# Optimization experiments

Measured on AMD Instinct MI355X. Metric: run time of the kernel, lower is better.

## Reference

```python
import jax, jax.numpy as jnp
import numpy as np

BATCH, DIM, L, N = 2, 768, 2048, 16


def setup_inputs() -> dict:
    key = jax.random.key(0)
    ks = jax.random.split(key, 8)
    u = jax.random.normal(ks[0], (BATCH, DIM, L), dtype=jnp.float32)
    delta = jax.random.uniform(ks[1], (BATCH, DIM, L), dtype=jnp.float32)
    # A must be negative for a stable SSM (exp(delta*A) <= 1)
    A = -jax.random.uniform(ks[2], (DIM, N), dtype=jnp.float32, minval=0.5, maxval=1.5)
    B = jax.random.normal(ks[3], (BATCH, N, L), dtype=jnp.float32)
    C = jax.random.normal(ks[4], (BATCH, N, L), dtype=jnp.float32)
    D = jax.random.normal(ks[5], (DIM,), dtype=jnp.float32)
    z = jax.random.normal(ks[6], (BATCH, DIM, L), dtype=jnp.float32)
    delta_bias = 0.1 * jax.random.normal(ks[7], (DIM,), dtype=jnp.float32)
    return {"u": u, "delta": delta, "A": A, "B": B, "C": C,
            "D": D, "z": z, "delta_bias": delta_bias}


def _selective_scan(u, delta, A, B, C, D, z, delta_bias):
    # delta_softplus=True path of mamba_ssm selective_scan_fn
    delta = jax.nn.softplus(delta + delta_bias[None, :, None])  # (b, d, l)
    # discretize: deltaA = exp(delta * A), deltaB_u = delta * B * u
    deltaA = jnp.exp(jnp.einsum('bdl,dn->lbdn', delta, A))          # (l, b, d, n)
    deltaBu = jnp.einsum('bdl,bnl,bdl->lbdn', delta, B, u)          # (l, b, d, n)
    C_t = jnp.transpose(C, (2, 0, 1))                               # (l, b, n)

    def step(x, inp):
        a, bu, c = inp
        x = a * x + bu                                              # (b, d, n)
        y = jnp.einsum('bdn,bn->bd', x, c)                          # (b, d)
        return x, y

    x0 = jnp.zeros((BATCH, DIM, N), dtype=u.dtype)
    _, ys = jax.lax.scan(step, x0, (deltaA, deltaBu, C_t))          # ys: (l, b, d)
    y = jnp.transpose(ys, (1, 2, 0))                                # (b, d, l)
    out = y + u * D[None, :, None]
    out = out * jax.nn.silu(z)
    return out


def reference(u, delta, A, B, C, D, z, delta_bias):
    return _selective_scan(u, delta, A, B, C, D, z, delta_bias)
```

## Files before the change

### kernel.cpp

```cpp
#include <hip/hip_runtime.h>


#define LOG2E 1.4426950408889634f
#define LN2   0.6931471805599453f

constexpr int BATCH = 2, DIM = 768, L = 2048, N = 16;
constexpr int NC = 128, LC = 16;
constexpr int DG = DIM / 64;
constexpr int CPB = 4;
constexpr int CG = NC / CPB;
constexpr int NBLK = BATCH * DG * CG;
constexpr int NCOMB = BATCH * DIM * N;
static_assert(NC * LC == L, "chunking must cover L");

__device__ __forceinline__ float fexp2(float x) { return __builtin_amdgcn_exp2f(x); }
__device__ __forceinline__ float softplus(float v) {
  float s = LN2 * __log2f(1.0f + fexp2(v * LOG2E));
  return (v > 20.0f) ? v : s;
}
__device__ __forceinline__ float silu(float v) { return v / (1.0f + fexp2(-v * LOG2E)); }

__global__ __launch_bounds__(256, 6) void k_pass1(
    const float* __restrict__ u, const float* __restrict__ delta,
    const float* __restrict__ A, const float* __restrict__ dbias,
    const float* __restrict__ Bg, float* __restrict__ h, float* __restrict__ S)
{
  __shared__ float slab[64][68];
  __shared__ float Bsr[64][20];

  const int bid = blockIdx.x, t = threadIdx.x;
  const int cgi = bid & 31;
  const int dgb = bid >> 5;
  const int dg = dgb % DG;
  const int b = dgb / DG;
  const int d0 = dg * 64, l0 = cgi * 64;

  const int w = t >> 6, lane = t & 63;
  const int c = cgi * CPB + w;
  const int d = d0 + lane;
  const int row16 = t >> 4;
  const int col4 = (t & 15) * 4;

#pragma unroll
  for (int rr = 0; rr < 4; rr++) {
    int row = row16 + rr * 16;
    long gof = ((long)(b * DIM + d0 + row)) * L + l0 + col4;
    *(float4*)&slab[row][col4] = *(const float4*)(delta + gof);
  }
  {
    long bof = ((long)(b * N + row16)) * L + l0 + col4;
    float4 v = *(const float4*)(Bg + bof);
    Bsr[col4 + 0][row16] = v.x;
    Bsr[col4 + 1][row16] = v.y;
    Bsr[col4 + 2][row16] = v.z;
    Bsr[col4 + 3][row16] = v.w;
  }

  float A2[N];
#pragma unroll
  for (int q = 0; q < 4; q++) {
    float4 av = *(const float4*)(A + d * N + q * 4);
    A2[q*4+0] = av.x * LOG2E; A2[q*4+1] = av.y * LOG2E;
    A2[q*4+2] = av.z * LOG2E; A2[q*4+3] = av.w * LOG2E;
  }
  const float bias = dbias[d];

  __syncthreads();

  float sp[LC], Ssum = 0.f;
#pragma unroll
  for (int q = 0; q < 4; q++) {
    float4 dv = *(const float4*)&slab[lane][w * LC + q * 4];
    sp[q*4+0] = softplus(dv.x + bias);
    sp[q*4+1] = softplus(dv.y + bias);
    sp[q*4+2] = softplus(dv.z + bias);
    sp[q*4+3] = softplus(dv.w + bias);
  }
#pragma unroll
  for (int j = 0; j < LC; j++) Ssum += sp[j];

  __syncthreads();

#pragma unroll
  for (int rr = 0; rr < 4; rr++) {
    int row = row16 + rr * 16;
    long gof = ((long)(b * DIM + d0 + row)) * L + l0 + col4;
    *(float4*)&slab[row][col4] = *(const float4*)(u + gof);
  }

  __syncthreads();

  float uu[LC];
#pragma unroll
  for (int q = 0; q < 4; q++) {
    float4 uv = *(const float4*)&slab[lane][w * LC + q * 4];
    uu[q*4+0] = uv.x; uu[q*4+1] = uv.y; uu[q*4+2] = uv.z; uu[q*4+3] = uv.w;
  }

  float x[N];
#pragma unroll
  for (int n = 0; n < N; n++) x[n] = 0.f;
#pragma unroll
  for (int j = 0; j < LC; j++) {
    const int row = w * LC + j;
    float bb[16];
#pragma unroll
    for (int q = 0; q < 4; q++) {
      float4 bv = *(const float4*)&Bsr[row][q * 4];
      bb[q*4+0] = bv.x; bb[q*4+1] = bv.y; bb[q*4+2] = bv.z; bb[q*4+3] = bv.w;
    }
    float du = sp[j] * uu[j];
#pragma unroll
    for (int n = 0; n < N; n++) {
      float a = fexp2(sp[j] * A2[n]);
      x[n] = a * x[n] + du * bb[n];
    }
  }

  const long hb = (((long)(b * NC + c)) * DIM + d) * N;
#pragma unroll
  for (int q = 0; q < 4; q++) {
    float4 v; v.x = x[q*4+0]; v.y = x[q*4+1]; v.z = x[q*4+2]; v.w = x[q*4+3];
    *(float4*)(h + hb + q * 4) = v;
  }
  S[(b * NC + c) * DIM + d] = Ssum;
}

__global__ __launch_bounds__(128) void k_pass2(
    const float* __restrict__ h, const float* __restrict__ S,
    const float* __restrict__ A, float* __restrict__ hI)
{
  int g = blockIdx.x * 128 + threadIdx.x;
  int n = g & 15;
  int r = g >> 4;
  int dd = r % DIM;
  int bb = r / DIM;
  const float a2 = A[dd * N + n] * LOG2E;
  const long step = (long)DIM * N;
  const long base0 = (((long)bb * NC) * DIM + dd) * N + n;
  const long sbase = (long)(bb * NC) * DIM + dd;

  float x = 0.f;
  for (int cb = 0; cb < NC / 16; cb++) {
    float hc[16], Sc[16];
#pragma unroll
    for (int k = 0; k < 16; k++) {
      hc[k] = h[base0 + (long)(cb * 16 + k) * step];
      Sc[k] = S[sbase + (long)(cb * 16 + k) * DIM];
    }
#pragma unroll
    for (int k = 0; k < 16; k++) {
      hI[base0 + (long)(cb * 16 + k) * step] = x;
      x = fexp2(Sc[k] * a2) * x + hc[k];
    }
  }
}

__global__ __launch_bounds__(256, 5) void k_pass3(
    const float* __restrict__ u, const float* __restrict__ delta,
    const float* __restrict__ A, const float* __restrict__ dbias,
    const float* __restrict__ Bg, const float* __restrict__ Cg,
    const float* __restrict__ Dv, const float* __restrict__ z,
    const float* __restrict__ xinit, float* __restrict__ out)
{
  __shared__ float slab[64][68];
  __shared__ float Bsr[64][20];
  __shared__ float Csr[64][20];

  const int bid = blockIdx.x, t = threadIdx.x;
  const int cgi = bid & 31;
  const int dgb = bid >> 5;
  const int dg = dgb % DG;
  const int b = dgb / DG;
  const int d0 = dg * 64, l0 = cgi * 64;

  const int w = t >> 6, lane = t & 63;
  const int c = cgi * CPB + w;
  const int d = d0 + lane;
  const int row16 = t >> 4;
  const int col4 = (t & 15) * 4;

#pragma unroll
  for (int rr = 0; rr < 4; rr++) {
    int row = row16 + rr * 16;
    long gof = ((long)(b * DIM + d0 + row)) * L + l0 + col4;
    *(float4*)&slab[row][col4] = *(const float4*)(delta + gof);
  }
  {
    long bof = ((long)(b * N + row16)) * L + l0 + col4;
    float4 v = *(const float4*)(Bg + bof);
    Bsr[col4 + 0][row16] = v.x;
    Bsr[col4 + 1][row16] = v.y;
    Bsr[col4 + 2][row16] = v.z;
    Bsr[col4 + 3][row16] = v.w;
    float4 wv = *(const float4*)(Cg + bof);
    Csr[col4 + 0][row16] = wv.x;
    Csr[col4 + 1][row16] = wv.y;
    Csr[col4 + 2][row16] = wv.z;
    Csr[col4 + 3][row16] = wv.w;
  }

  float A2[N];
#pragma unroll
  for (int q = 0; q < 4; q++) {
    float4 av = *(const float4*)(A + d * N + q * 4);
    A2[q*4+0] = av.x * LOG2E; A2[q*4+1] = av.y * LOG2E;
    A2[q*4+2] = av.z * LOG2E; A2[q*4+3] = av.w * LOG2E;
  }
  const float bias = dbias[d];

  const long hb = (((long)(b * NC + c)) * DIM + d) * N;
  float x[N];
#pragma unroll
  for (int q = 0; q < 4; q++) {
    float4 v = *(const float4*)(xinit + hb + q * 4);
    x[q*4+0] = v.x; x[q*4+1] = v.y; x[q*4+2] = v.z; x[q*4+3] = v.w;
  }

  __syncthreads();

  float sp[LC];
#pragma unroll
  for (int q = 0; q < 4; q++) {
    float4 dv = *(const float4*)&slab[lane][w * LC + q * 4];
    sp[q*4+0] = softplus(dv.x + bias);
    sp[q*4+1] = softplus(dv.y + bias);
    sp[q*4+2] = softplus(dv.z + bias);
    sp[q*4+3] = softplus(dv.w + bias);
  }

  __syncthreads();

#pragma unroll
  for (int rr = 0; rr < 4; rr++) {
    int row = row16 + rr * 16;
    long gof = ((long)(b * DIM + d0 + row)) * L + l0 + col4;
    *(float4*)&slab[row][col4] = *(const float4*)(u + gof);
  }

  __syncthreads();

  float uu[LC];
#pragma unroll
  for (int q = 0; q < 4; q++) {
    float4 uv = *(const float4*)&slab[lane][w * LC + q * 4];
    uu[q*4+0] = uv.x; uu[q*4+1] = uv.y; uu[q*4+2] = uv.z; uu[q*4+3] = uv.w;
  }

  float y[LC];
#pragma unroll
  for (int j = 0; j < LC; j++) {
    const int row = w * LC + j;
    float bb[16], ccv[16];
#pragma unroll
    for (int q = 0; q < 4; q++) {
      float4 bv = *(const float4*)&Bsr[row][q * 4];
      float4 cv = *(const float4*)&Csr[row][q * 4];
      bb[q*4+0] = bv.x; bb[q*4+1] = bv.y; bb[q*4+2] = bv.z; bb[q*4+3] = bv.w;
      ccv[q*4+0] = cv.x; ccv[q*4+1] = cv.y; ccv[q*4+2] = cv.z; ccv[q*4+3] = cv.w;
    }
    float du = sp[j] * uu[j];
    float acc = 0.f;
#pragma unroll
    for (int n = 0; n < N; n++) {
      float a = fexp2(sp[j] * A2[n]);
      x[n] = a * x[n] + du * bb[n];
      acc += x[n] * ccv[n];
    }
    y[j] = acc;
  }

#pragma unroll
  for (int q = 0; q < 4; q++) {
    float4 v; v.x = y[q*4+0]; v.y = y[q*4+1]; v.z = y[q*4+2]; v.w = y[q*4+3];
    *(float4*)&slab[lane][w * LC + q * 4] = v;
  }

  __syncthreads();

#pragma unroll
  for (int rr = 0; rr < 4; rr++) {
    int row = row16 + rr * 16;
    long gof = ((long)(b * DIM + d0 + row)) * L + l0 + col4;
    float4 zv = *(const float4*)(z + gof);
    float4 uv = *(const float4*)(u + gof);
    float4 yv = *(const float4*)&slab[row][col4];
    float Dd2 = Dv[d0 + row];
    float4 ov;
    ov.x = (yv.x + uv.x * Dd2) * silu(zv.x);
    ov.y = (yv.y + uv.y * Dd2) * silu(zv.y);
    ov.z = (yv.z + uv.z * Dd2) * silu(zv.z);
    ov.w = (yv.w + uv.w * Dd2) * silu(zv.w);
    *(float4*)(out + gof) = ov;
  }
}

__global__ __launch_bounds__(256) void k_simple(
    const float* __restrict__ u, const float* __restrict__ delta,
    const float* __restrict__ A, const float* __restrict__ dbias,
    const float* __restrict__ Bm, const float* __restrict__ Cm,
    const float* __restrict__ Dv, const float* __restrict__ z,
    float* __restrict__ out) {
  int t = blockIdx.x * 256 + threadIdx.x;
  int n = t % N;
  int bd = t / N;
  int d = bd % DIM;
  int b = bd / DIM;
  float A2 = A[d * N + n] * LOG2E;
  float bias = dbias[d];
  float Dd = Dv[d];
  const float* Bp = Bm + ((long)b * N + n) * L;
  const float* Cp = Cm + ((long)b * N + n) * L;
  long base = (long)bd * L;
  float x = 0.0f;
  for (int l = 0; l < L; l++) {
    float dv = delta[base + l];
    float uv = u[base + l];
    float sp = softplus(dv + bias);
    float a = fexp2(sp * A2);
    x = a * x + sp * uv * Bp[l];
    float y = x * Cp[l];
#pragma unroll
    for (int off = 8; off; off >>= 1) y += __shfl_xor(y, off, 16);
    if (n == 0) {
      float zv = z[base + l];
      out[base + l] = (y + uv * Dd) * silu(zv);
    }
  }
}

extern "C" void kernel_launch(void* const* d_in, const int* in_sizes, int n_in,
                              void* d_out, int out_size, void* d_ws, size_t ws_size,
                              hipStream_t stream) {
  const float* u     = (const float*)d_in[0];
  const float* delta = (const float*)d_in[1];
  const float* A     = (const float*)d_in[2];
  const float* Bm    = (const float*)d_in[3];
  const float* Cm    = (const float*)d_in[4];
  const float* Dv    = (const float*)d_in[5];
  const float* z     = (const float*)d_in[6];
  const float* dbias = (const float*)d_in[7];
  float* out = (float*)d_out;

  const size_t hp  = (size_t)BATCH * NC * DIM * N;
  const size_t spn = (size_t)BATCH * NC * DIM;
  const size_t need = (2 * hp + spn) * sizeof(float);

  if (ws_size < need) {
    k_simple<<<(BATCH * DIM * N) / 256, 256, 0, stream>>>(u, delta, A, dbias, Bm, Cm, Dv, z, out);
    return;
  }

  float* h  = (float*)d_ws;
  float* S  = h + hp;
  float* hI = S + spn;

  k_pass1<<<NBLK, 256, 0, stream>>>(u, delta, A, dbias, Bm, h, S);
  k_pass2<<<NCOMB / 128, 128, 0, stream>>>(h, S, A, hI);
  k_pass3<<<NBLK, 256, 0, stream>>>(u, delta, A, dbias, Bm, Cm, Dv, z, hI, out);
}
```

Before: 132.6 us.

## Issue all global loads up front into registers and use separate delta/u LDS tiles

Both pass1 and pass3 now issue the delta, u, B (and C, z, xinit in pass3) global loads together into registers before writing them to LDS. Delta and u get separate padded shared tiles, which removes one round of barrier-separated load/compute phases. Pass3 also reuses u from LDS and z from registers in the epilogue instead of re-reading them from global memory. The cost is more registers and LDS per block, and the launch-bound occupancy hint drops to 3 blocks per CU.

```diff
diff --git a/kernel.cpp b/kernel.cpp
--- a/kernel.cpp
+++ b/kernel.cpp
@@ -11,6 +11,7 @@
 constexpr int CG = NC / CPB;
 constexpr int NBLK = BATCH * DG * CG;
 constexpr int NCOMB = BATCH * DIM * N;
+constexpr int PAD = 76;
 static_assert(NC * LC == L, "chunking must cover L");
 
 __device__ __forceinline__ float fexp2(float x) { return __builtin_amdgcn_exp2f(x); }
@@ -20,12 +21,13 @@
 }
 __device__ __forceinline__ float silu(float v) { return v / (1.0f + fexp2(-v * LOG2E)); }
 
-__global__ __launch_bounds__(256, 6) void k_pass1(
+__global__ __launch_bounds__(256, 3) void k_pass1(
     const float* __restrict__ u, const float* __restrict__ delta,
     const float* __restrict__ A, const float* __restrict__ dbias,
     const float* __restrict__ Bg, float* __restrict__ h, float* __restrict__ S)
 {
-  __shared__ float slab[64][68];
+  __shared__ float ds_[64][PAD];
+  __shared__ float us[64][PAD];
   __shared__ float Bsr[64][20];
 
   const int bid = blockIdx.x, t = threadIdx.x;
@@ -41,20 +43,16 @@
   const int row16 = t >> 4;
   const int col4 = (t & 15) * 4;
 
+  float4 dreg[4], ureg[4];
 #pragma unroll
   for (int rr = 0; rr < 4; rr++) {
     int row = row16 + rr * 16;
     long gof = ((long)(b * DIM + d0 + row)) * L + l0 + col4;
-    *(float4*)&slab[row][col4] = *(const float4*)(delta + gof);
-  }
-  {
-    long bof = ((long)(b * N + row16)) * L + l0 + col4;
-    float4 v = *(const float4*)(Bg + bof);
-    Bsr[col4 + 0][row16] = v.x;
-    Bsr[col4 + 1][row16] = v.y;
-    Bsr[col4 + 2][row16] = v.z;
-    Bsr[col4 + 3][row16] = v.w;
-  }
+    dreg[rr] = *(const float4*)(delta + gof);
+    ureg[rr] = *(const float4*)(u + gof);
+  }
+  long bof = ((long)(b * N + row16)) * L + l0 + col4;
+  float4 breg = *(const float4*)(Bg + bof);
 
   float A2[N];
 #pragma unroll
@@ -65,37 +63,31 @@
   }
   const float bias = dbias[d];
 
+#pragma unroll
+  for (int rr = 0; rr < 4; rr++) {
+    int row = row16 + rr * 16;
+    *(float4*)&ds_[row][col4] = dreg[rr];
+    *(float4*)&us[row][col4]  = ureg[rr];
+  }
+  Bsr[col4 + 0][row16] = breg.x;
+  Bsr[col4 + 1][row16] = breg.y;
+  Bsr[col4 + 2][row16] = breg.z;
+  Bsr[col4 + 3][row16] = breg.w;
+
   __syncthreads();
 
-  float sp[LC], Ssum = 0.f;
-#pragma unroll
-  for (int q = 0; q < 4; q++) {
-    float4 dv = *(const float4*)&slab[lane][w * LC + q * 4];
-    sp[q*4+0] = softplus(dv.x + bias);
-    sp[q*4+1] = softplus(dv.y + bias);
-    sp[q*4+2] = softplus(dv.z + bias);
-    sp[q*4+3] = softplus(dv.w + bias);
+  float sp[LC], uu[LC], Ssum = 0.f;
+#pragma unroll
+  for (int q = 0; q < 4; q++) {
+    float4 dv = *(const float4*)&ds_[lane][w * LC + q * 4];
+    float4 uv = *(const float4*)&us[lane][w * LC + q * 4];
+    sp[q*4+0] = softplus(dv.x + bias); uu[q*4+0] = uv.x;
+    sp[q*4+1] = softplus(dv.y + bias); uu[q*4+1] = uv.y;
+    sp[q*4+2] = softplus(dv.z + bias); uu[q*4+2] = uv.z;
+    sp[q*4+3] = softplus(dv.w + bias); uu[q*4+3] = uv.w;
   }
 #pragma unroll
   for (int j = 0; j < LC; j++) Ssum += sp[j];
-
-  __syncthreads();
-
-#pragma unroll
-  for (int rr = 0; rr < 4; rr++) {
-    int row = row16 + rr * 16;
-    long gof = ((long)(b * DIM + d0 + row)) * L + l0 + col4;
-    *(float4*)&slab[row][col4] = *(const float4*)(u + gof);
-  }
-
-  __syncthreads();
-
-  float uu[LC];
-#pragma unroll
-  for (int q = 0; q < 4; q++) {
-    float4 uv = *(const float4*)&slab[lane][w * LC + q * 4];
-    uu[q*4+0] = uv.x; uu[q*4+1] = uv.y; uu[q*4+2] = uv.z; uu[q*4+3] = uv.w;
-  }
 
   float x[N];
 #pragma unroll
@@ -156,14 +148,15 @@
   }
 }
 
-__global__ __launch_bounds__(256, 5) void k_pass3(
+__global__ __launch_bounds__(256, 3) void k_pass3(
     const float* __restrict__ u, const float* __restrict__ delta,
     const float* __restrict__ A, const float* __restrict__ dbias,
     const float* __restrict__ Bg, const float* __restrict__ Cg,
     const float* __restrict__ Dv, const float* __restrict__ z,
     const float* __restrict__ xinit, float* __restrict__ out)
 {
-  __shared__ float slab[64][68];
+  __shared__ float ds_[64][PAD];
+  __shared__ float us[64][PAD];
   __shared__ float Bsr[64][20];
   __shared__ float Csr[64][20];
 
@@ -180,24 +173,25 @@
   const int row16 = t >> 4;
   const int col4 = (t & 15) * 4;
 
+  float4 dreg[4], ureg[4], zreg[4];
 #pragma unroll
   for (int rr = 0; rr < 4; rr++) {
     int row = row16 + rr * 16;
     long gof = ((long)(b * DIM + d0 + row)) * L + l0 + col4;
-    *(float4*)&slab[row][col4] = *(const float4*)(delta + gof);
-  }
-  {
-    long bof = ((long)(b * N + row16)) * L + l0 + col4;
-    float4 v = *(const float4*)(Bg + bof);
-    Bsr[col4 + 0][row16] = v.x;
-    Bsr[col4 + 1][row16] = v.y;
-    Bsr[col4 + 2][row16] = v.z;
-    Bsr[col4 + 3][row16] = v.w;
-    float4 wv = *(const float4*)(Cg + bof);
-    Csr[col4 + 0][row16] = wv.x;
-    Csr[col4 + 1][row16] = wv.y;
-    Csr[col4 + 2][row16] = wv.z;
-    Csr[col4 + 3][row16] = wv.w;
+    dreg[rr] = *(const float4*)(delta + gof);
+    ureg[rr] = *(const float4*)(u + gof);
+    zreg[rr] = *(const float4*)(z + gof);
+  }
+  long bof = ((long)(b * N + row16)) * L + l0 + col4;
+  float4 breg = *(const float4*)(Bg + bof);
+  float4 creg = *(const float4*)(Cg + bof);
+
+  const long hb = (((long)(b * NC + c)) * DIM + d) * N;
+  float x[N];
+#pragma unroll
+  for (int q = 0; q < 4; q++) {
+    float4 v = *(const float4*)(xinit + hb + q * 4);
+    x[q*4+0] = v.x; x[q*4+1] = v.y; x[q*4+2] = v.z; x[q*4+3] = v.w;
   }
 
   float A2[N];
@@ -209,42 +203,32 @@
   }
   const float bias = dbias[d];
 
-  const long hb = (((long)(b * NC + c)) * DIM + d) * N;
-  float x[N];
-#pragma unroll
-  for (int q = 0; q < 4; q++) {
-    float4 v = *(const float4*)(xinit + hb + q * 4);
-    x[q*4+0] = v.x; x[q*4+1] = v.y; x[q*4+2] = v.z; x[q*4+3] = v.w;
-  }
+#pragma unroll
+  for (int rr = 0; rr < 4; rr++) {
+    int row = row16 + rr * 16;
+    *(float4*)&ds_[row][col4] = dreg[rr];
+    *(float4*)&us[row][col4]  = ureg[rr];
+  }
+  Bsr[col4 + 0][row16] = breg.x;
+  Bsr[col4 + 1][row16] = breg.y;
+  Bsr[col4 + 2][row16] = breg.z;
+  Bsr[col4 + 3][row16] = breg.w;
+  Csr[col4 + 0][row16] = creg.x;
+  Csr[col4 + 1][row16] = creg.y;
+  Csr[col4 + 2][row16] = creg.z;
+  Csr[col4 + 3][row16] = creg.w;
 
   __syncthreads();
 
-  float sp[LC];
-#pragma unroll
-  for (int q = 0; q < 4; q++) {
-    float4 dv = *(const float4*)&slab[lane][w * LC + q * 4];
-    sp[q*4+0] = softplus(dv.x + bias);
-    sp[q*4+1] = softplus(dv.y + bias);
-    sp[q*4+2] = softplus(dv.z + bias);
-    sp[q*4+3] = softplus(dv.w + bias);
-  }
-
-  __syncthreads();
-
-#pragma unroll
-  for (int rr = 0; rr < 4; rr++) {
-    int row = row16 + rr * 16;
-    long gof = ((long)(b * DIM + d0 + row)) * L + l0 + col4;
-    *(float4*)&slab[row][col4] = *(const float4*)(u + gof);
-  }
-
-  __syncthreads();
-
-  float uu[LC];
-#pragma unroll
-  for (int q = 0; q < 4; q++) {
-    float4 uv = *(const float4*)&slab[lane][w * LC + q * 4];
-    uu[q*4+0] = uv.x; uu[q*4+1] = uv.y; uu[q*4+2] = uv.z; uu[q*4+3] = uv.w;
+  float sp[LC], uu[LC];
+#pragma unroll
+  for (int q = 0; q < 4; q++) {
+    float4 dv = *(const float4*)&ds_[lane][w * LC + q * 4];
+    float4 uv = *(const float4*)&us[lane][w * LC + q * 4];
+    sp[q*4+0] = softplus(dv.x + bias); uu[q*4+0] = uv.x;
+    sp[q*4+1] = softplus(dv.y + bias); uu[q*4+1] = uv.y;
+    sp[q*4+2] = softplus(dv.z + bias); uu[q*4+2] = uv.z;
+    sp[q*4+3] = softplus(dv.w + bias); uu[q*4+3] = uv.w;
   }
 
   float y[LC];
@@ -270,10 +254,11 @@
     y[j] = acc;
   }
 
+  __syncthreads();
 #pragma unroll
   for (int q = 0; q < 4; q++) {
     float4 v; v.x = y[q*4+0]; v.y = y[q*4+1]; v.z = y[q*4+2]; v.w = y[q*4+3];
-    *(float4*)&slab[lane][w * LC + q * 4] = v;
+    *(float4*)&ds_[lane][w * LC + q * 4] = v;
   }
 
   __syncthreads();
@@ -282,9 +267,9 @@
   for (int rr = 0; rr < 4; rr++) {
     int row = row16 + rr * 16;
     long gof = ((long)(b * DIM + d0 + row)) * L + l0 + col4;
-    float4 zv = *(const float4*)(z + gof);
-    float4 uv = *(const float4*)(u + gof);
-    float4 yv = *(const float4*)&slab[row][col4];
+    float4 zv = zreg[rr];
+    float4 yv = *(const float4*)&ds_[row][col4];
+    float4 uv = *(const float4*)&us[row][col4];
     float Dd2 = Dv[d0 + row];
     float4 ov;
     ov.x = (yv.x + uv.x * Dd2) * silu(zv.x);
```

After: 131.2 us. No clear change (-1.1%).
